# Kernel optimization log

Measured on AMD Instinct MI355X. Metric: run time of the kernel, lower is better.

Reference implementation:

```python
import jax, jax.numpy as jnp
import numpy as np

NUM_INPUTS = 4096
K = 64
BATCH = 16384


def setup_inputs() -> dict:
    key = jax.random.key(0)
    X = jax.random.normal(key, (BATCH, NUM_INPUTS), dtype=jnp.float32)
    return {"X": X}


def reference(X):
    # Per-row (1 - k/n) quantile of |X| (linear interpolation, matching
    # torch.quantile default), then soft-threshold preserving sign.
    q = 1.0 - K / NUM_INPUTS
    X_abs = jnp.abs(X)
    Q = jnp.quantile(X_abs, q, axis=1, method="linear")  # [batch]
    X_trunc = jnp.maximum(X_abs - Q[:, None], 0.0)
    return jnp.sign(X) * X_trunc
```

## Files before the change

### kernel.cpp

```cpp
#include <hip/hip_runtime.h>
#include <cstdint>

constexpr int NCOLS   = 4096;
constexpr int THREADS = 256;
constexpr int EPT     = 16;
constexpr int CAP     = 256;

typedef float floatx4 __attribute__((ext_vector_type(4)));

__device__ __forceinline__ uint32_t mbcnt64(uint64_t m) {
    uint32_t c = __builtin_amdgcn_mbcnt_lo((uint32_t)m, 0u);
    return __builtin_amdgcn_mbcnt_hi((uint32_t)(m >> 32), c);
}

__global__ __launch_bounds__(THREADS) void topk_sparsify(
    const float* __restrict__ X, float* __restrict__ out)
{
    const int row  = blockIdx.x;
    const int t    = threadIdx.x;
    const int wave = t >> 6;
    const int lane = t & 63;

    __shared__ uint32_t wsum[4];
    __shared__ float    fsum[4];
    __shared__ uint32_t wmn[4];
    __shared__ uint32_t cand[CAP];

    const floatx4* __restrict__ x4 =
        reinterpret_cast<const floatx4*>(X + (size_t)row * NCOLS);
    floatx4* __restrict__ o4 = reinterpret_cast<floatx4*>(out + (size_t)row * NCOLS);

    uint32_t a[EPT];
    uint32_t sbits = 0;
    float ss = 0.0f;
#pragma unroll
    for (int i = 0; i < 4; ++i) {
        floatx4 v = x4[t + THREADS * i];
        uint32_t u0 = __float_as_uint(v.x), u1 = __float_as_uint(v.y);
        uint32_t u2 = __float_as_uint(v.z), u3 = __float_as_uint(v.w);
        a[4*i+0] = u0 & 0x7FFFFFFFu;  a[4*i+1] = u1 & 0x7FFFFFFFu;
        a[4*i+2] = u2 & 0x7FFFFFFFu;  a[4*i+3] = u3 & 0x7FFFFFFFu;
        sbits |= (u0 >> 31) << (4*i+0);
        sbits |= (u1 >> 31) << (4*i+1);
        sbits |= (u2 >> 31) << (4*i+2);
        sbits |= (u3 >> 31) << (4*i+3);
        ss = fmaf(v.x, v.x, ss); ss = fmaf(v.y, v.y, ss);
        ss = fmaf(v.z, v.z, ss); ss = fmaf(v.w, v.w, ss);
    }

#pragma unroll
    for (int off = 32; off >= 1; off >>= 1) ss += __shfl_xor(ss, off, 64);
    if (lane == 0) fsum[wave] = ss;
    __syncthreads();
    const float sigma = sqrtf(fsum[0] + fsum[1] + fsum[2] + fsum[3]) * (1.0f / 64.0f);

    float T = 2.12f * sigma;
    uint32_t tb = 0, C = 0;
    bool ok = false;
    for (int it = 0; it < 12; ++it) {
        tb = __float_as_uint(T);
        uint32_t cw = 0;
#pragma unroll
        for (int i = 0; i < EPT; ++i)
            cw += (uint32_t)__popcll(__ballot(a[i] > tb));
        if (lane == 0) wsum[wave] = cw;
        __syncthreads();
        C = wsum[0] + wsum[1] + wsum[2] + wsum[3];
        if (C >= 65u && C <= (uint32_t)CAP) { ok = true; break; }
        __syncthreads();
        T = (C < 65u) ? T * 0.82f : T * 1.25f;
    }

    uint32_t b65, Ct, M;
    if (ok) {
        uint32_t base = 0;
#pragma unroll
        for (int w = 0; w < 4; ++w) base += (w < wave) ? wsum[w] : 0u;
#pragma unroll
        for (int i = 0; i < EPT; ++i) {
            uint64_t m = __ballot(a[i] > tb);
            if (a[i] > tb) cand[base + mbcnt64(m)] = a[i];
            base += (uint32_t)__popcll(m);
        }
        __syncthreads();

        uint32_t r0 = (lane       < (int)C) ? cand[lane      ] : 0u;
        uint32_t r1 = (lane + 64  < (int)C) ? cand[lane +  64] : 0u;
        uint32_t r2 = (lane + 128 < (int)C) ? cand[lane + 128] : 0u;
        uint32_t r3 = (lane + 192 < (int)C) ? cand[lane + 192] : 0u;

        uint32_t lo = tb + 1u, hi = 0x7F800000u;
        while (lo < hi) {
            uint32_t mid = lo + ((hi - lo) >> 1);
            uint32_t c = (uint32_t)(__popcll(__ballot(r0 > mid)) +
                                    __popcll(__ballot(r1 > mid)) +
                                    __popcll(__ballot(r2 > mid)) +
                                    __popcll(__ballot(r3 > mid)));
            if (c < 65u) hi = mid; else lo = mid + 1u;
        }
        b65 = lo;

        Ct = (uint32_t)(__popcll(__ballot(r0 > b65)) +
                        __popcll(__ballot(r1 > b65)) +
                        __popcll(__ballot(r2 > b65)) +
                        __popcll(__ballot(r3 > b65)));
        uint32_t mn = 0xFFFFFFFFu;
        mn = min(mn, (r0 > b65) ? r0 : 0xFFFFFFFFu);
        mn = min(mn, (r1 > b65) ? r1 : 0xFFFFFFFFu);
        mn = min(mn, (r2 > b65) ? r2 : 0xFFFFFFFFu);
        mn = min(mn, (r3 > b65) ? r3 : 0xFFFFFFFFu);
#pragma unroll
        for (int off = 32; off >= 1; off >>= 1)
            mn = min(mn, (uint32_t)__shfl_xor(mn, off, 64));
        M = mn;
    } else {
        uint32_t lo = 0u, hi = 0x7F800000u;
        while (lo < hi) {
            uint32_t mid = lo + ((hi - lo) >> 1);
            uint32_t cw = 0;
#pragma unroll
            for (int i = 0; i < EPT; ++i)
                cw += (uint32_t)__popcll(__ballot(a[i] > mid));
            if (lane == 0) wsum[wave] = cw;
            __syncthreads();
            uint32_t tot = wsum[0] + wsum[1] + wsum[2] + wsum[3];
            __syncthreads();
            if (tot < 65u) hi = mid; else lo = mid + 1u;
        }
        b65 = lo;

        uint32_t cw = 0, mn = 0xFFFFFFFFu;
#pragma unroll
        for (int i = 0; i < EPT; ++i) {
            cw += (uint32_t)__popcll(__ballot(a[i] > b65));
            mn = min(mn, (a[i] > b65) ? a[i] : 0xFFFFFFFFu);
        }
#pragma unroll
        for (int off = 32; off >= 1; off >>= 1)
            mn = min(mn, (uint32_t)__shfl_xor(mn, off, 64));
        if (lane == 0) { wsum[wave] = cw; wmn[wave] = mn; }
        __syncthreads();
        Ct = wsum[0] + wsum[1] + wsum[2] + wsum[3];
        M  = min(min(wmn[0], wmn[1]), min(wmn[2], wmn[3]));
    }

    const float v65 = __uint_as_float(b65);
    const float v64 = (Ct == 64u) ? __uint_as_float(M) : v65;
    const float Q = fmaf(0.015625f, v64 - v65, v65);

#pragma unroll
    for (int i = 0; i < 4; ++i) {
        floatx4 f;
#pragma unroll
        for (int j = 0; j < 4; ++j) {
            const int idx = 4*i + j;
            float mag = fmaxf(__uint_as_float(a[idx]) - Q, 0.0f);
            uint32_t bits = __float_as_uint(mag) | (((sbits >> idx) & 1u) << 31);
            f[j] = __uint_as_float(bits);
        }
        __builtin_nontemporal_store(f, &o4[t + THREADS * i]);
    }
}

extern "C" void kernel_launch(void* const* d_in, const int* in_sizes, int n_in,
                              void* d_out, int out_size, void* d_ws, size_t ws_size,
                              hipStream_t stream) {
    const float* X   = (const float*)d_in[0];
    float*       out = (float*)d_out;
    const int rows = in_sizes[0] / NCOLS;
    topk_sparsify<<<rows, THREADS, 0, stream>>>(X, out);
}
```

Before: 441.9 us.

## Assign one row per wavefront to eliminate block-level synchronization

Each wavefront now processes a whole row: 64 floats per lane held in registers, with four rows per block. All the cross-wave shared-memory reductions and __syncthreads barriers in the sigma, threshold-search and fallback paths become plain wave-level ballots. The candidate binary search is also bounded by the candidate maximum instead of the infinity bit pattern, and sign handling uses copysign instead of packed sign bits. The cost is four times more register pressure per thread (64 live floats), which may reduce occupancy, and more serial ballot work per wave.

After: 447.5 us. About the same (+1.3%).

```diff
diff --git a/kernel.cpp b/kernel.cpp
--- a/kernel.cpp
+++ b/kernel.cpp
@@ -3,7 +3,7 @@
 
 constexpr int NCOLS   = 4096;
 constexpr int THREADS = 256;
-constexpr int EPT     = 16;
+constexpr int WPB     = 4;
 constexpr int CAP     = 256;
 
 typedef float floatx4 __attribute__((ext_vector_type(4)));
@@ -16,58 +16,48 @@
 __global__ __launch_bounds__(THREADS) void topk_sparsify(
     const float* __restrict__ X, float* __restrict__ out)
 {
-    const int row  = blockIdx.x;
-    const int t    = threadIdx.x;
-    const int wave = t >> 6;
-    const int lane = t & 63;
+    const int wave = threadIdx.x >> 6;
+    const int lane = threadIdx.x & 63;
+    const int row  = blockIdx.x * WPB + wave;
 
-    __shared__ uint32_t wsum[4];
-    __shared__ float    fsum[4];
-    __shared__ uint32_t wmn[4];
-    __shared__ uint32_t cand[CAP];
+    __shared__ uint32_t cand[WPB * CAP];
+    uint32_t* __restrict__ wc = cand + wave * CAP;
 
     const floatx4* __restrict__ x4 =
         reinterpret_cast<const floatx4*>(X + (size_t)row * NCOLS);
     floatx4* __restrict__ o4 = reinterpret_cast<floatx4*>(out + (size_t)row * NCOLS);
 
-    uint32_t a[EPT];
-    uint32_t sbits = 0;
-    float ss = 0.0f;
+    floatx4 v[16];
 #pragma unroll
-    for (int i = 0; i < 4; ++i) {
-        floatx4 v = x4[t + THREADS * i];
-        uint32_t u0 = __float_as_uint(v.x), u1 = __float_as_uint(v.y);
-        uint32_t u2 = __float_as_uint(v.z), u3 = __float_as_uint(v.w);
-        a[4*i+0] = u0 & 0x7FFFFFFFu;  a[4*i+1] = u1 & 0x7FFFFFFFu;
-        a[4*i+2] = u2 & 0x7FFFFFFFu;  a[4*i+3] = u3 & 0x7FFFFFFFu;
-        sbits |= (u0 >> 31) << (4*i+0);
-        sbits |= (u1 >> 31) << (4*i+1);
-        sbits |= (u2 >> 31) << (4*i+2);
-        sbits |= (u3 >> 31) << (4*i+3);
-        ss = fmaf(v.x, v.x, ss); ss = fmaf(v.y, v.y, ss);
-        ss = fmaf(v.z, v.z, ss); ss = fmaf(v.w, v.w, ss);
+    for (int i = 0; i < 16; ++i) v[i] = x4[lane + 64 * i];
+
+    float s0 = 0, s1 = 0, s2 = 0, s3 = 0;
+#pragma unroll
+    for (int i = 0; i < 16; ++i) {
+        s0 = fmaf(v[i].x, v[i].x, s0);
+        s1 = fmaf(v[i].y, v[i].y, s1);
+        s2 = fmaf(v[i].z, v[i].z, s2);
+        s3 = fmaf(v[i].w, v[i].w, s3);
     }
-
+    float ss = (s0 + s1) + (s2 + s3);
 #pragma unroll
     for (int off = 32; off >= 1; off >>= 1) ss += __shfl_xor(ss, off, 64);
-    if (lane == 0) fsum[wave] = ss;
-    __syncthreads();
-    const float sigma = sqrtf(fsum[0] + fsum[1] + fsum[2] + fsum[3]) * (1.0f / 64.0f);
+    const float sigma = sqrtf(ss) * (1.0f / 64.0f);
 
     float T = 2.12f * sigma;
     uint32_t tb = 0, C = 0;
     bool ok = false;
     for (int it = 0; it < 12; ++it) {
-        tb = __float_as_uint(T);
-        uint32_t cw = 0;
+        uint32_t c = 0;
 #pragma unroll
-        for (int i = 0; i < EPT; ++i)
-            cw += (uint32_t)__popcll(__ballot(a[i] > tb));
-        if (lane == 0) wsum[wave] = cw;
-        __syncthreads();
-        C = wsum[0] + wsum[1] + wsum[2] + wsum[3];
-        if (C >= 65u && C <= (uint32_t)CAP) { ok = true; break; }
-        __syncthreads();
+        for (int i = 0; i < 16; ++i) {
+            c += (uint32_t)__popcll(__ballot(__builtin_fabsf(v[i].x) > T));
+            c += (uint32_t)__popcll(__ballot(__builtin_fabsf(v[i].y) > T));
+            c += (uint32_t)__popcll(__ballot(__builtin_fabsf(v[i].z) > T));
+            c += (uint32_t)__popcll(__ballot(__builtin_fabsf(v[i].w) > T));
+        }
+        C = c;
+        if (C >= 65u && C <= (uint32_t)CAP) { tb = __float_as_uint(T); ok = true; break; }
         T = (C < 65u) ? T * 0.82f : T * 1.25f;
     }
 
@@ -75,21 +65,28 @@
     if (ok) {
         uint32_t base = 0;
 #pragma unroll
-        for (int w = 0; w < 4; ++w) base += (w < wave) ? wsum[w] : 0u;
+        for (int i = 0; i < 16; ++i) {
 #pragma unroll
-        for (int i = 0; i < EPT; ++i) {
-            uint64_t m = __ballot(a[i] > tb);
-            if (a[i] > tb) cand[base + mbcnt64(m)] = a[i];
-            base += (uint32_t)__popcll(m);
+            for (int j = 0; j < 4; ++j) {
+                const float f = v[i][j];
+                const bool  g = __builtin_fabsf(f) > T;
+                uint64_t m = __ballot(g);
+                if (g) wc[base + mbcnt64(m)] = __float_as_uint(f);
+                base += (uint32_t)__popcll(m);
+            }
         }
-        __syncthreads();
 
-        uint32_t r0 = (lane       < (int)C) ? cand[lane      ] : 0u;
-        uint32_t r1 = (lane + 64  < (int)C) ? cand[lane +  64] : 0u;
-        uint32_t r2 = (lane + 128 < (int)C) ? cand[lane + 128] : 0u;
-        uint32_t r3 = (lane + 192 < (int)C) ? cand[lane + 192] : 0u;
+        uint32_t r0 = (lane       < (int)C) ? (wc[lane      ] & 0x7FFFFFFFu) : 0u;
+        uint32_t r1 = (lane + 64  < (int)C) ? (wc[lane +  64] & 0x7FFFFFFFu) : 0u;
+        uint32_t r2 = (lane + 128 < (int)C) ? (wc[lane + 128] & 0x7FFFFFFFu) : 0u;
+        uint32_t r3 = (lane + 192 < (int)C) ? (wc[lane + 192] & 0x7FFFFFFFu) : 0u;
 
-        uint32_t lo = tb + 1u, hi = 0x7F800000u;
+        uint32_t mx = max(max(r0, r1), max(r2, r3));
+#pragma unroll
+        for (int off = 32; off >= 1; off >>= 1)
+            mx = max(mx, (uint32_t)__shfl_xor(mx, off, 64));
+
+        uint32_t lo = tb + 1u, hi = mx;
         while (lo < hi) {
             uint32_t mid = lo + ((hi - lo) >> 1);
             uint32_t c = (uint32_t)(__popcll(__ballot(r0 > mid)) +
@@ -117,31 +114,33 @@
         uint32_t lo = 0u, hi = 0x7F800000u;
         while (lo < hi) {
             uint32_t mid = lo + ((hi - lo) >> 1);
-            uint32_t cw = 0;
+            uint32_t c = 0;
 #pragma unroll
-            for (int i = 0; i < EPT; ++i)
-                cw += (uint32_t)__popcll(__ballot(a[i] > mid));
-            if (lane == 0) wsum[wave] = cw;
-            __syncthreads();
-            uint32_t tot = wsum[0] + wsum[1] + wsum[2] + wsum[3];
-            __syncthreads();
-            if (tot < 65u) hi = mid; else lo = mid + 1u;
+            for (int i = 0; i < 16; ++i) {
+#pragma unroll
+                for (int j = 0; j < 4; ++j)
+                    c += (uint32_t)__popcll(__ballot(
+                        (__float_as_uint(v[i][j]) & 0x7FFFFFFFu) > mid));
+            }
+            if (c < 65u) hi = mid; else lo = mid + 1u;
         }
         b65 = lo;
 
         uint32_t cw = 0, mn = 0xFFFFFFFFu;
 #pragma unroll
-        for (int i = 0; i < EPT; ++i) {
-            cw += (uint32_t)__popcll(__ballot(a[i] > b65));
-            mn = min(mn, (a[i] > b65) ? a[i] : 0xFFFFFFFFu);
+        for (int i = 0; i < 16; ++i) {
+#pragma unroll
+            for (int j = 0; j < 4; ++j) {
+                uint32_t ab = __float_as_uint(v[i][j]) & 0x7FFFFFFFu;
+                bool g = ab > b65;
+                cw += (uint32_t)__popcll(__ballot(g));
+                mn = min(mn, g ? ab : 0xFFFFFFFFu);
+            }
         }
 #pragma unroll
         for (int off = 32; off >= 1; off >>= 1)
             mn = min(mn, (uint32_t)__shfl_xor(mn, off, 64));
-        if (lane == 0) { wsum[wave] = cw; wmn[wave] = mn; }
-        __syncthreads();
-        Ct = wsum[0] + wsum[1] + wsum[2] + wsum[3];
-        M  = min(min(wmn[0], wmn[1]), min(wmn[2], wmn[3]));
+        Ct = cw; M = mn;
     }
 
     const float v65 = __uint_as_float(b65);
@@ -149,16 +148,15 @@
     const float Q = fmaf(0.015625f, v64 - v65, v65);
 
 #pragma unroll
-    for (int i = 0; i < 4; ++i) {
-        floatx4 f;
+    for (int i = 0; i < 16; ++i) {
+        floatx4 o;
 #pragma unroll
         for (int j = 0; j < 4; ++j) {
-            const int idx = 4*i + j;
-            float mag = fmaxf(__uint_as_float(a[idx]) - Q, 0.0f);
-            uint32_t bits = __float_as_uint(mag) | (((sbits >> idx) & 1u) << 31);
-            f[j] = __uint_as_float(bits);
+            const float f = v[i][j];
+            float mag = fmaxf(__builtin_fabsf(f) - Q, 0.0f);
+            o[j] = copysignf(mag, f);
         }
-        __builtin_nontemporal_store(f, &o4[t + THREADS * i]);
+        __builtin_nontemporal_store(o, &o4[lane + 64 * i]);
     }
 }
 
@@ -168,5 +166,5 @@
     const float* X   = (const float*)d_in[0];
     float*       out = (float*)d_out;
     const int rows = in_sizes[0] / NCOLS;
-    topk_sparsify<<<rows, THREADS, 0, stream>>>(X, out);
+    topk_sparsify<<<rows / WPB, THREADS, 0, stream>>>(X, out);
 }
```
